# Kernel optimization log

Hardware: AMD Instinct MI355X
Metric: run time of the kernel (lower is better)

## Reference

```python
import jax, jax.numpy as jnp
import numpy as np

ANNEAL_T_START = 5.0
T_END = 1.0


def setup_inputs() -> dict:
    key = jax.random.key(0)
    ks = jax.random.split(key, 8)
    B, V, H, CD, WID = 8192, 1024, 128, 16, 64
    return {
        "cond": jax.random.normal(ks[0], (B, CD), jnp.float32),
        "W": 0.01 * jax.random.normal(ks[1], (V, H), jnp.float32),
        "b": 0.01 * jax.random.normal(ks[2], (V,), jnp.float32),
        "c": 0.01 * jax.random.normal(ks[3], (H,), jnp.float32),
        "fc1_w": jax.random.normal(ks[4], (WID, CD), jnp.float32) / np.float32(np.sqrt(CD)),
        "fc1_b": jnp.zeros((WID,), jnp.float32),
        "fc2_w": jax.random.normal(ks[5], (2 * (V + H), WID), jnp.float32) / np.float32(np.sqrt(WID)),
        "fc2_b": jnp.zeros((2 * (V + H),), jnp.float32),
        "falloff": jnp.float32(1.0),
        "steps": 16,
    }


def _bern(key, p):
    # Bernoulli sample as float of same dtype as p.
    return (jax.random.uniform(key, p.shape, p.dtype) < p).astype(p.dtype)


def reference(cond, W, b, c, fc1_w, fc1_b, fc2_w, fc2_b, falloff, steps):
    V, H = W.shape
    B = cond.shape[0]
    dtype = W.dtype

    # Conditioner: FiLM-style modulation of visible/hidden biases.
    x = jnp.tanh(cond @ fc1_w.T + fc1_b)
    x = x @ fc2_w.T + fc2_b  # [B, 2*(V+H)]
    gamma_b = x[:, :V]
    beta_b = x[:, V:2 * V]
    gamma_c = x[:, 2 * V:2 * V + H]
    beta_c = x[:, 2 * V + H:]
    b_mod = (1.0 + gamma_b) * b + beta_b  # [B, V]
    c_mod = (1.0 + gamma_c) * c + beta_c  # [B, H]
    bsum = jnp.sum(b_mod, axis=-1)  # [B], constant across steps

    # Annealing temperature schedule (sigmoid falloff).
    t = jnp.arange(steps, dtype=dtype)
    s = 1.0 / (1.0 + jnp.exp(falloff * (t - steps / 2.0)))
    temps = T_END + (ANNEAL_T_START - T_END) * s  # [steps]

    base = jax.random.key(42)
    v0 = _bern(jax.random.fold_in(base, 2 ** 20), jnp.full((B, V), 0.5, dtype))
    s0_0 = jnp.ones((B, 1), dtype)

    def flip(v, s0):
        return s0 * v + (1.0 - s0) * (1.0 - v)

    def step(carry, xs):
        v, s0 = carry
        i, T = xs
        k1, k2, k3 = jax.random.split(jax.random.fold_in(base, i), 3)
        v_eff = flip(v, s0)
        p_h = jax.nn.sigmoid((v_eff @ W + c_mod) / T)  # [B, H]
        h = _bern(k1, p_h)
        a = h @ W.T  # [B, V]
        vb = jnp.sum(v * b_mod, axis=-1)
        va = jnp.sum(v * a, axis=-1)
        dE = -bsum - jnp.sum(a, axis=-1) + 2.0 * vb + 2.0 * va  # [B]
        p_s0 = jax.nn.sigmoid(dE / T)
        s0n = _bern(k2, p_s0)[:, None]  # [B, 1]
        p_v = jax.nn.sigmoid((a + b_mod) / T)
        v_samp = _bern(k3, p_v)
        v_next = flip(v_samp, s0n)
        return (v_next, s0n), None

    (v, _), _ = jax.lax.scan(
        step, (v0, s0_0), (jnp.arange(steps, dtype=jnp.int32), temps)
    )
    return v
```

## Files before the change

kernel.cpp:

```cpp
#include <hip/hip_runtime.h>
#include <stdint.h>

#pragma clang fp contract(off)

#define B_ 8192
#define V_ 1024
#define H_ 128
#define CD_ 16
#define WID_ 64
#define NOUT_ 2304
#define STEPS_ 16

typedef float f32x2 __attribute__((ext_vector_type(2)));

__device__ __forceinline__ void pkfma(f32x2& acc, f32x2 wv, f32x2 bf2) {
  asm("v_pk_fma_f32 %0, %1, %2, %0" : "+v"(acc) : "v"(wv), "v"(bf2));
}

__host__ __device__ __forceinline__ void tf2x32(uint32_t k0, uint32_t k1,
                                                uint32_t x0, uint32_t x1,
                                                uint32_t* o0, uint32_t* o1) {
  uint32_t ks2 = k0 ^ k1 ^ 0x1BD11BDAu;
#define RL_(v, d) (((v) << (d)) | ((v) >> (32 - (d))))
#define RND_(a) { x0 += x1; x1 = RL_(x1, a); x1 ^= x0; }
  x0 += k0; x1 += k1;
  RND_(13) RND_(15) RND_(26) RND_(6)
  x0 += k1; x1 += ks2 + 1u;
  RND_(17) RND_(29) RND_(16) RND_(24)
  x0 += ks2; x1 += k0 + 2u;
  RND_(13) RND_(15) RND_(26) RND_(6)
  x0 += k0; x1 += k1 + 3u;
  RND_(17) RND_(29) RND_(16) RND_(24)
  x0 += k1; x1 += ks2 + 4u;
  RND_(13) RND_(15) RND_(26) RND_(6)
  x0 += ks2; x1 += k0 + 5u;
#undef RND_
#undef RL_
  *o0 = x0; *o1 = x1;
}

struct Keys { uint32_t a[6]; };

__device__ __forceinline__ uint32_t draw_bits(uint32_t ka, uint32_t kb, uint32_t j) {
  uint32_t x0, x1;
  tf2x32(ka, kb, 0u, j, &x0, &x1);
  return x0 ^ x1;
}

__device__ __forceinline__ float bits_to_u(uint32_t bits) {
  return __fsub_rn(__uint_as_float((bits >> 9) | 0x3f800000u), 1.0f);
}

__device__ __forceinline__ float exp_a(float x) {
  float xc = fminf(fmaxf(x, -88.3762626647949f), 88.3762626647950f);
  float fx = floorf(__fadd_rn(__fmul_rn(xc, 1.44269504088896341f), 0.5f));
  float xr = __fsub_rn(xc, __fmul_rn(0.693359375f, fx));
  xr = __fsub_rn(xr, __fmul_rn(-2.12194440e-4f, fx));
  float zz = __fmul_rn(xr, xr);
  float y = 1.9875691500E-4f;
  y = __fadd_rn(__fmul_rn(y, xr), 1.3981999507E-3f);
  y = __fadd_rn(__fmul_rn(y, xr), 8.3334519073E-3f);
  y = __fadd_rn(__fmul_rn(y, xr), 4.1665795894E-2f);
  y = __fadd_rn(__fmul_rn(y, xr), 1.6666665459E-1f);
  y = __fadd_rn(__fmul_rn(y, xr), 5.0000001201E-1f);
  y = __fadd_rn(__fmul_rn(y, zz), xr);
  y = __fadd_rn(y, 1.0f);
  int n = (int)fx;
  float sc = __int_as_float((n + 127) << 23);
  return __fmul_rn(y, sc);
}

__device__ __forceinline__ float tanh_a(float xin) {
  float x = fmaxf(fminf(xin, 7.90531110763549805f), -7.90531110763549805f);
  float x2 = __fmul_rn(x, x);
  float p = __fadd_rn(__fmul_rn(x2, -2.76076847742355e-16f), 2.00018790482477e-13f);
  p = __fadd_rn(__fmul_rn(x2, p), -8.60467152213735e-11f);
  p = __fadd_rn(__fmul_rn(x2, p), 5.12229709037114e-08f);
  p = __fadd_rn(__fmul_rn(x2, p), 1.48572235717979e-05f);
  p = __fadd_rn(__fmul_rn(x2, p), 6.37261928875436e-04f);
  p = __fadd_rn(__fmul_rn(x2, p), 4.89352455891786e-03f);
  p = __fmul_rn(x, p);
  float q = __fadd_rn(__fmul_rn(x2, 1.19825839466702e-06f), 1.18534705686654e-04f);
  q = __fadd_rn(__fmul_rn(x2, q), 2.26843463243900e-03f);
  q = __fadd_rn(__fmul_rn(x2, q), 4.89352518554385e-03f);
  float r = p / q;
  if (fabsf(xin) < 0.0004f) r = xin;
  return r;
}

__device__ __forceinline__ float sigmoid_a(float z) {
  float e = exp_a(-z);
  return 1.0f / __fadd_rn(1.0f, e);
}

__global__ void k_transpose(const float* __restrict__ W, float* __restrict__ WT,
                            const float* __restrict__ fc2w, float* __restrict__ fc2T) {
  int i = blockIdx.x * blockDim.x + threadIdx.x;
  if (i < V_ * H_) { int v = i / H_, h = i % H_; WT[h * V_ + v] = W[i]; }
  if (i < NOUT_ * WID_) { int j = i / WID_, w = i % WID_; fc2T[w * NOUT_ + j] = fc2w[i]; }
}

__global__ void k_temps(const float* __restrict__ falloff, float* __restrict__ temps) {
  int t = threadIdx.x;
  if (t < 16) {
    float arg = __fmul_rn(*falloff, __fsub_rn((float)t, 8.0f));
    float e = exp_a(arg);
    float s = 1.0f / __fadd_rn(1.0f, e);
    temps[t] = __fadd_rn(1.0f, __fmul_rn(4.0f, s));
  }
}

__global__ void k_mlp1(const float* __restrict__ cond, const float* __restrict__ fc1w,
                       const float* __restrict__ fc1b, float* __restrict__ xout) {
  int idx = blockIdx.x * blockDim.x + threadIdx.x;
  if (idx >= B_ * WID_) return;
  int row = idx >> 6, w = idx & 63;
  float acc = 0.0f;
  for (int k = 0; k < CD_; k++) acc = __fmaf_rn(cond[row * CD_ + k], fc1w[w * CD_ + k], acc);
  float z = __fadd_rn(acc, fc1b[w]);
  xout[idx] = tanh_a(z);
}

__global__ __launch_bounds__(128) void k_mlp2b(const float* __restrict__ xmlp,
                       const float* __restrict__ fc2T, const float* __restrict__ fc2b,
                       const float* __restrict__ bvec, float* __restrict__ b_mod) {
  __shared__ float xs[32][WID_];
  int jbase = blockIdx.x * 128;
  int r0 = blockIdx.y * 32;
  int tid = threadIdx.x;
  for (int t = tid; t < 32 * WID_; t += 128)
    xs[t >> 6][t & 63] = xmlp[(r0 + (t >> 6)) * WID_ + (t & 63)];
  __syncthreads();
  int j = jbase + tid;
  float accg[32], accb[32];
#pragma unroll
  for (int r = 0; r < 32; r++) { accg[r] = 0.0f; accb[r] = 0.0f; }
  for (int w = 0; w < WID_; w++) {
    float fg = fc2T[w * NOUT_ + j];
    float fb = fc2T[w * NOUT_ + 1024 + j];
#pragma unroll
    for (int r = 0; r < 32; r++) {
      float xv = xs[r][w];
      accg[r] = __fmaf_rn(xv, fg, accg[r]);
      accb[r] = __fmaf_rn(xv, fb, accb[r]);
    }
  }
  float bj = bvec[j];
  float biasg = fc2b[j], biasb = fc2b[1024 + j];
#pragma unroll
  for (int r = 0; r < 32; r++) {
    float g = __fadd_rn(accg[r], biasg);
    float bb = __fadd_rn(accb[r], biasb);
    float t1 = __fadd_rn(1.0f, g);
    b_mod[(r0 + r) * V_ + j] = __fadd_rn(__fmul_rn(t1, bj), bb);
  }
}

__global__ __launch_bounds__(128) void k_mlp2c(const float* __restrict__ xmlp,
                       const float* __restrict__ fc2T, const float* __restrict__ fc2b,
                       const float* __restrict__ cvec, float* __restrict__ c_mod) {
  __shared__ float xs[32][WID_];
  int r0 = blockIdx.y * 32;
  int tid = threadIdx.x;
  for (int t = tid; t < 32 * WID_; t += 128)
    xs[t >> 6][t & 63] = xmlp[(r0 + (t >> 6)) * WID_ + (t & 63)];
  __syncthreads();
  float accg[32], accb[32];
#pragma unroll
  for (int r = 0; r < 32; r++) { accg[r] = 0.0f; accb[r] = 0.0f; }
  for (int w = 0; w < WID_; w++) {
    float fg = fc2T[w * NOUT_ + 2048 + tid];
    float fb = fc2T[w * NOUT_ + 2176 + tid];
#pragma unroll
    for (int r = 0; r < 32; r++) {
      float xv = xs[r][w];
      accg[r] = __fmaf_rn(xv, fg, accg[r]);
      accb[r] = __fmaf_rn(xv, fb, accb[r]);
    }
  }
  float cj = cvec[tid];
  float biasg = fc2b[2048 + tid], biasb = fc2b[2176 + tid];
#pragma unroll
  for (int r = 0; r < 32; r++) {
    float g = __fadd_rn(accg[r], biasg);
    float bb = __fadd_rn(accb[r], biasb);
    float t1 = __fadd_rn(1.0f, g);
    c_mod[(r0 + r) * H_ + tid] = __fadd_rn(__fmul_rn(t1, cj), bb);
  }
}

__global__ __launch_bounds__(64) void k_bsum(const float* __restrict__ b_mod,
                                             float* __restrict__ bsum) {
  int row = blockIdx.x * 64 + threadIdx.x;
  const float4* bp = (const float4*)(b_mod + (size_t)row * V_);
  float acc = 0.0f;
  for (int c = 0; c < 32; c++) {
    float4 Bv[8];
#pragma unroll
    for (int q = 0; q < 8; q++) Bv[q] = bp[c * 8 + q];
#pragma unroll
    for (int q = 0; q < 8; q++) {
      acc = __fadd_rn(acc, Bv[q].x);
      acc = __fadd_rn(acc, Bv[q].y);
      acc = __fadd_rn(acc, Bv[q].z);
      acc = __fadd_rn(acc, Bv[q].w);
    }
  }
  bsum[row] = acc;
}

__global__ void k_v0(float* __restrict__ vout, uint32_t* __restrict__ v_bits,
                     float* __restrict__ s0, uint32_t kva, uint32_t kvb) {
  int idx = blockIdx.x * blockDim.x + threadIdx.x;
  int row = idx >> 10, col = idx & 1023;
  uint32_t bits = draw_bits(kva, kvb, (uint32_t)idx);
  float u = bits_to_u(bits);
  float v = (u < 0.5f) ? 1.0f : 0.0f;
  vout[idx] = v;
  unsigned long long m = __ballot(v == 1.0f);
  if ((threadIdx.x & 63) == 0) {
    v_bits[row * 32 + (col >> 5)] = (uint32_t)m;
    v_bits[row * 32 + (col >> 5) + 1] = (uint32_t)(m >> 32);
  }
  if (col == 0) s0[row] = 1.0f;
}

__global__ __launch_bounds__(256) void k_h(const float* __restrict__ W,
                   const float* __restrict__ c_mod, const uint32_t* __restrict__ v_bits,
                   const float* __restrict__ s0, uint32_t* __restrict__ h_bits,
                   const float* __restrict__ temps, int step, Keys kn) {
  __shared__ uint32_t nib[16][32];
  int tid = threadIdx.x;
  int ct = tid & 31;
  int rt = tid >> 5;
  int h0 = ct << 2;
  int row0 = blockIdx.x * 16 + rt * 2;
  float T = temps[step];
  f32x2 a00 = {0.f, 0.f}, a01 = {0.f, 0.f};
  f32x2 a10 = {0.f, 0.f}, a11 = {0.f, 0.f};
  uint32_t flip0 = (s0[row0] == 0.0f) ? 0xFFFFFFFFu : 0u;
  uint32_t flip1 = (s0[row0 + 1] == 0.0f) ? 0xFFFFFFFFu : 0u;
  const float* wp = W + h0;
  const uint4* vb0q = (const uint4*)(v_bits + (size_t)row0 * 32);
  const uint4* vb1q = (const uint4*)(v_bits + (size_t)(row0 + 1) * 32);

  float4 A[8], Bq[8];
  uint32_t m0, m1;
  auto LOADW = [&](float4* d, int kbase) {
#pragma unroll
    for (int i = 0; i < 8; i++)
      d[i] = *(const float4*)(wp + (size_t)(kbase + i) * H_);
  };
  auto DO8 = [&](const float4* wv) {
#pragma unroll
    for (int j = 0; j < 8; j++) {
      uint32_t s0m = (uint32_t)((int32_t)m0 >> 31); m0 <<= 1;
      uint32_t s1m = (uint32_t)((int32_t)m1 >> 31); m1 <<= 1;
      float bf0 = __uint_as_float(s0m & 0x3f800000u);
      float bf1 = __uint_as_float(s1m & 0x3f800000u);
      f32x2 wlo = {wv[j].x, wv[j].y};
      f32x2 whi = {wv[j].z, wv[j].w};
      f32x2 b0 = {bf0, bf0};
      f32x2 b1 = {bf1, bf1};
      pkfma(a00, wlo, b0); pkfma(a01, whi, b0);
      pkfma(a10, wlo, b1); pkfma(a11, whi, b1);
    }
  };

  uint4 q0 = vb0q[0], q1 = vb1q[0];
  uint4 q0n, q1n;
  LOADW(A, 0);
  for (int kq = 0; kq < 8; kq++) {
    if (kq < 7) { q0n = vb0q[kq + 1]; q1n = vb1q[kq + 1]; }
    const uint32_t w0s[4] = {q0.x, q0.y, q0.z, q0.w};
    const uint32_t w1s[4] = {q1.x, q1.y, q1.z, q1.w};
#pragma unroll
    for (int wq = 0; wq < 4; wq++) {
      int kb = kq * 128 + wq * 32;
      m0 = __brev(w0s[wq]) ^ flip0;
      m1 = __brev(w1s[wq]) ^ flip1;
      LOADW(Bq, kb + 8);  DO8(A);
      LOADW(A, kb + 16);  DO8(Bq);
      LOADW(Bq, kb + 24); DO8(A);
      if (kb + 32 < 1024) LOADW(A, kb + 32);
      DO8(Bq);
    }
    q0 = q0n; q1 = q1n;
  }

  const f32x2* accs[2][2] = {{&a00, &a01}, {&a10, &a11}};
#pragma unroll
  for (int r = 0; r < 2; r++) {
    int row = row0 + r;
    float4 cm = *(const float4*)(c_mod + (size_t)row * H_ + h0);
    const float cma[4] = {cm.x, cm.y, cm.z, cm.w};
    const float ac[4] = {(*accs[r][0])[0], (*accs[r][0])[1],
                         (*accs[r][1])[0], (*accs[r][1])[1]};
    uint32_t nb = 0;
#pragma unroll
    for (int e = 0; e < 4; e++) {
      float z = __fadd_rn(ac[e], cma[e]) / T;
      float p = sigmoid_a(z);
      uint32_t b = draw_bits(kn.a[0], kn.a[1], (uint32_t)(row * H_ + h0 + e));
      if (bits_to_u(b) < p) nb |= 1u << e;
    }
    nib[rt * 2 + r][ct] = nb;
  }
  __syncthreads();
  if (tid < 64) {
    int rloc = tid >> 2, wq = tid & 3;
    uint32_t word = 0;
#pragma unroll
    for (int i = 0; i < 8; i++) word |= nib[rloc][wq * 8 + i] << (4 * i);
    h_bits[(size_t)(blockIdx.x * 16 + rloc) * 4 + wq] = word;
  }
}

__global__ __launch_bounds__(256) void k_a(const float* __restrict__ WT,
                   const uint32_t* __restrict__ h_bits, float* __restrict__ a) {
  int tid = threadIdx.x;
  int ct = tid & 63;
  int rt = tid >> 6;
  int v0 = blockIdx.x * 256 + (ct << 2);
  int r0 = blockIdx.y * 32 + rt * 8;
  f32x2 acc[8][2];
#pragma unroll
  for (int r = 0; r < 8; r++) { acc[r][0] = f32x2{0.f, 0.f}; acc[r][1] = f32x2{0.f, 0.f}; }
  uint4 hw[8];
#pragma unroll
  for (int r = 0; r < 8; r++) hw[r] = *(const uint4*)(h_bits + (size_t)(r0 + r) * 4);
  const float* wp0 = WT + v0;

  auto asect = [&](int WW, const uint32_t mwin[8]) {
    uint32_t m[8];
#pragma unroll
    for (int r = 0; r < 8; r++) m[r] = __brev(mwin[r]);
    const float* wp = wp0 + (size_t)(WW * 32) * V_;
    for (int j4 = 0; j4 < 8; j4++) {
#pragma unroll
      for (int jj = 0; jj < 4; jj++) {
        float4 wv = *(const float4*)(wp + (size_t)jj * V_);
        f32x2 wlo = {wv.x, wv.y};
        f32x2 whi = {wv.z, wv.w};
#pragma unroll
        for (int r = 0; r < 8; r++) {
          uint32_t sm = (uint32_t)((int32_t)m[r] >> 31);
          m[r] <<= 1;
          float bf = __uint_as_float(sm & 0x3f800000u);
          f32x2 b2 = {bf, bf};
          pkfma(acc[r][0], wlo, b2);
          pkfma(acc[r][1], whi, b2);
        }
      }
      wp += (size_t)4 * V_;
    }
  };

  {
    uint32_t mw[8];
#pragma unroll
    for (int r = 0; r < 8; r++) mw[r] = hw[r].x;
    asect(0, mw);
#pragma unroll
    for (int r = 0; r < 8; r++) mw[r] = hw[r].y;
    asect(1, mw);
#pragma unroll
    for (int r = 0; r < 8; r++) mw[r] = hw[r].z;
    asect(2, mw);
#pragma unroll
    for (int r = 0; r < 8; r++) mw[r] = hw[r].w;
    asect(3, mw);
  }

#pragma unroll
  for (int r = 0; r < 8; r++) {
    float4 o = make_float4(acc[r][0][0], acc[r][0][1], acc[r][1][0], acc[r][1][1]);
    *(float4*)(a + (size_t)(r0 + r) * V_ + v0) = o;
  }
}

__global__ __launch_bounds__(256) void k_s0(const float* __restrict__ a,
                     const float* __restrict__ b_mod, const float* __restrict__ bsum,
                     const uint32_t* __restrict__ v_bits, float* __restrict__ s0,
                     const float* __restrict__ temps, int step, Keys kn) {
  __shared__ float As[2][16][132];
  __shared__ float Bs[2][16][132];
  int tid = threadIdx.x;
  int r0 = blockIdx.x * 16;

  auto STAGE = [&](int buf, int c) {
#pragma unroll
    for (int i = 0; i < 2; i++) {
      int e = tid + i * 256;
      int r = e >> 5, c4 = e & 31;
      float4 av = *(const float4*)(a + (size_t)(r0 + r) * V_ + c * 128 + c4 * 4);
      float4 bv = *(const float4*)(b_mod + (size_t)(r0 + r) * V_ + c * 128 + c4 * 4);
      *(float4*)&As[buf][r][c4 * 4] = av;
      *(float4*)&Bs[buf][r][c4 * 4] = bv;
    }
  };

  float suma = 0.0f, vb = 0.0f, va = 0.0f;
  STAGE(0, 0);
  __syncthreads();
  for (int c = 0; c < 8; c++) {
    if (c < 7) STAGE((c + 1) & 1, c + 1);
    if (tid < 16) {
      int row = r0 + tid;
      uint4 mw = *(const uint4*)(v_bits + (size_t)row * 32 + c * 4);
      const uint32_t mm[4] = {mw.x, mw.y, mw.z, mw.w};
#pragma unroll
      for (int w4 = 0; w4 < 4; w4++) {
        uint32_t m = mm[w4];
#pragma unroll
        for (int j4 = 0; j4 < 8; j4++) {
          float4 av4 = *(const float4*)&As[c & 1][tid][w4 * 32 + j4 * 4];
          float4 bv4 = *(const float4*)&Bs[c & 1][tid][w4 * 32 + j4 * 4];
          const float ax[4] = {av4.x, av4.y, av4.z, av4.w};
          const float bx[4] = {bv4.x, bv4.y, bv4.z, bv4.w};
#pragma unroll
          for (int e = 0; e < 4; e++) {
            float bit = (float)((m >> (j4 * 4 + e)) & 1u);
            suma = __fadd_rn(suma, ax[e]);
            vb = __fmaf_rn(bx[e], bit, vb);
            va = __fmaf_rn(ax[e], bit, va);
          }
        }
      }
    }
    __syncthreads();
  }
  if (tid < 16) {
    int row = r0 + tid;
    float dE = __fsub_rn(-bsum[row], suma);
    dE = __fadd_rn(dE, __fmul_rn(2.0f, vb));
    dE = __fadd_rn(dE, __fmul_rn(2.0f, va));
    float T = temps[step];
    float p = sigmoid_a(dE / T);
    uint32_t bits = draw_bits(kn.a[2], kn.a[3], (uint32_t)row);
    float u = bits_to_u(bits);
    s0[row] = (u < p) ? 1.0f : 0.0f;
  }
}

__global__ void k_v(const float* __restrict__ a, const float* __restrict__ b_mod,
                    const float* __restrict__ s0, float* __restrict__ vout,
                    uint32_t* __restrict__ v_bits, const float* __restrict__ temps, int step,
                    Keys kn) {
  int idx = blockIdx.x * blockDim.x + threadIdx.x;
  int row = idx >> 10, col = idx & 1023;
  float T = temps[step];
  float z = __fadd_rn(a[idx], b_mod[idx]) / T;
  float p = sigmoid_a(z);
  uint32_t bits = draw_bits(kn.a[4], kn.a[5], (uint32_t)idx);
  float u = bits_to_u(bits);
  float vs = (u < p) ? 1.0f : 0.0f;
  float vn = (s0[row] != 0.0f) ? vs : (1.0f - vs);
  vout[idx] = vn;
  unsigned long long m = __ballot(vn == 1.0f);
  if ((threadIdx.x & 63) == 0) {
    v_bits[row * 32 + (col >> 5)] = (uint32_t)m;
    v_bits[row * 32 + (col >> 5) + 1] = (uint32_t)(m >> 32);
  }
}

extern "C" void kernel_launch(void* const* d_in, const int* in_sizes, int n_in,
                              void* d_out, int out_size, void* d_ws, size_t ws_size,
                              hipStream_t stream) {
  const float* cond = (const float*)d_in[0];
  const float* W = (const float*)d_in[1];
  const float* bvec = (const float*)d_in[2];
  const float* cvec = (const float*)d_in[3];
  const float* fc1w = (const float*)d_in[4];
  const float* fc1b = (const float*)d_in[5];
  const float* fc2w = (const float*)d_in[6];
  const float* fc2b = (const float*)d_in[7];
  const float* falloff = (const float*)d_in[8];
  float* out = (float*)d_out;

  char* ws = (char*)d_ws;
  size_t off = 0;
  auto alloc = [&](size_t bytes) { void* p = ws + off; off += (bytes + 255) & ~(size_t)255; return p; };
  float* b_mod = (float*)alloc((size_t)B_ * V_ * 4);
  float* c_mod = (float*)alloc((size_t)B_ * H_ * 4);
  float* abuf  = (float*)alloc((size_t)B_ * V_ * 4);
  float* xmlp  = (float*)alloc((size_t)B_ * WID_ * 4);
  float* bsum  = (float*)alloc((size_t)B_ * 4);
  float* s0    = (float*)alloc((size_t)B_ * 4);
  uint32_t* v_bits = (uint32_t*)alloc((size_t)B_ * 32 * 4);
  uint32_t* h_bits = (uint32_t*)alloc((size_t)B_ * 4 * 4);
  float* WT    = (float*)alloc((size_t)H_ * V_ * 4);
  float* fc2T  = (float*)alloc((size_t)WID_ * NOUT_ * 4);
  float* temps = (float*)alloc(16 * 4);

  uint32_t kva, kvb;
  tf2x32(0u, 42u, 0u, 1048576u, &kva, &kvb);
  Keys kn[16];
  for (int i = 0; i < 16; i++) {
    uint32_t f0, f1;
    tf2x32(0u, 42u, 0u, (uint32_t)i, &f0, &f1);
    uint32_t a0, a1;
    tf2x32(f0, f1, 0u, 0u, &a0, &a1); kn[i].a[0] = a0; kn[i].a[1] = a1;
    tf2x32(f0, f1, 0u, 1u, &a0, &a1); kn[i].a[2] = a0; kn[i].a[3] = a1;
    tf2x32(f0, f1, 0u, 2u, &a0, &a1); kn[i].a[4] = a0; kn[i].a[5] = a1;
  }

  k_transpose<<<(NOUT_ * WID_ + 255) / 256, 256, 0, stream>>>(W, WT, fc2w, fc2T);
  k_temps<<<1, 64, 0, stream>>>(falloff, temps);
  k_mlp1<<<(B_ * WID_) / 256, 256, 0, stream>>>(cond, fc1w, fc1b, xmlp);
  k_mlp2b<<<dim3(8, 256), 128, 0, stream>>>(xmlp, fc2T, fc2b, bvec, b_mod);
  k_mlp2c<<<dim3(1, 256), 128, 0, stream>>>(xmlp, fc2T, fc2b, cvec, c_mod);
  k_bsum<<<B_ / 64, 64, 0, stream>>>(b_mod, bsum);
  k_v0<<<(B_ * V_) / 256, 256, 0, stream>>>(out, v_bits, s0, kva, kvb);

  for (int i = 0; i < STEPS_; i++) {
    k_h<<<B_ / 16, 256, 0, stream>>>(W, c_mod, v_bits, s0, h_bits, temps, i, kn[i]);
    k_a<<<dim3(4, B_ / 32), 256, 0, stream>>>(WT, h_bits, abuf);
    k_s0<<<B_ / 16, 256, 0, stream>>>(abuf, b_mod, bsum, v_bits, s0, temps, i, kn[i]);
    k_v<<<(B_ * V_) / 256, 256, 0, stream>>>(abuf, b_mod, s0, out, v_bits, temps, i, kn[i]);
  }
}
```

Measured before the change: 2.989 ms.

## Keep raw sampled visible bits, defer flip, write float output once

```diff
diff --git a/kernel.cpp b/kernel.cpp
--- a/kernel.cpp
+++ b/kernel.cpp
@@ -209,15 +209,13 @@
   bsum[row] = acc;
 }
 
-__global__ void k_v0(float* __restrict__ vout, uint32_t* __restrict__ v_bits,
-                     float* __restrict__ s0, uint32_t kva, uint32_t kvb) {
+__global__ void k_v0(uint32_t* __restrict__ v_bits, float* __restrict__ s0,
+                     uint32_t kva, uint32_t kvb) {
   int idx = blockIdx.x * blockDim.x + threadIdx.x;
   int row = idx >> 10, col = idx & 1023;
   uint32_t bits = draw_bits(kva, kvb, (uint32_t)idx);
   float u = bits_to_u(bits);
-  float v = (u < 0.5f) ? 1.0f : 0.0f;
-  vout[idx] = v;
-  unsigned long long m = __ballot(v == 1.0f);
+  unsigned long long m = __ballot(u < 0.5f);
   if ((threadIdx.x & 63) == 0) {
     v_bits[row * 32 + (col >> 5)] = (uint32_t)m;
     v_bits[row * 32 + (col >> 5) + 1] = (uint32_t)(m >> 32);
@@ -227,8 +225,8 @@
 
 __global__ __launch_bounds__(256) void k_h(const float* __restrict__ W,
                    const float* __restrict__ c_mod, const uint32_t* __restrict__ v_bits,
-                   const float* __restrict__ s0, uint32_t* __restrict__ h_bits,
-                   const float* __restrict__ temps, int step, Keys kn) {
+                   uint32_t* __restrict__ h_bits, const float* __restrict__ temps,
+                   int step, Keys kn) {
   __shared__ uint32_t nib[16][32];
   int tid = threadIdx.x;
   int ct = tid & 31;
@@ -238,13 +236,11 @@
   float T = temps[step];
   f32x2 a00 = {0.f, 0.f}, a01 = {0.f, 0.f};
   f32x2 a10 = {0.f, 0.f}, a11 = {0.f, 0.f};
-  uint32_t flip0 = (s0[row0] == 0.0f) ? 0xFFFFFFFFu : 0u;
-  uint32_t flip1 = (s0[row0 + 1] == 0.0f) ? 0xFFFFFFFFu : 0u;
   const float* wp = W + h0;
   const uint4* vb0q = (const uint4*)(v_bits + (size_t)row0 * 32);
   const uint4* vb1q = (const uint4*)(v_bits + (size_t)(row0 + 1) * 32);
 
-  float4 A[8], Bq[8];
+  float4 W0[8], W1[8], W2[8], W3[8];
   uint32_t m0, m1;
   auto LOADW = [&](float4* d, int kbase) {
 #pragma unroll
@@ -266,27 +262,34 @@
       pkfma(a10, wlo, b1); pkfma(a11, whi, b1);
     }
   };
+  auto WQ = [&](int kb, uint32_t mw0, uint32_t mw1, bool l0, bool l1, bool l2) {
+    m0 = __brev(mw0);
+    m1 = __brev(mw1);
+    LOADW(W3, kb + 24); DO8(W0);
+    if (l0) LOADW(W0, kb + 32);
+    DO8(W1);
+    if (l1) LOADW(W1, kb + 40);
+    DO8(W2);
+    if (l2) LOADW(W2, kb + 48);
+    DO8(W3);
+  };
 
   uint4 q0 = vb0q[0], q1 = vb1q[0];
   uint4 q0n, q1n;
-  LOADW(A, 0);
-  for (int kq = 0; kq < 8; kq++) {
-    if (kq < 7) { q0n = vb0q[kq + 1]; q1n = vb1q[kq + 1]; }
+  LOADW(W0, 0); LOADW(W1, 8); LOADW(W2, 16);
+  for (int kq = 0; kq < 7; kq++) {
+    q0n = vb0q[kq + 1]; q1n = vb1q[kq + 1];
     const uint32_t w0s[4] = {q0.x, q0.y, q0.z, q0.w};
     const uint32_t w1s[4] = {q1.x, q1.y, q1.z, q1.w};
 #pragma unroll
-    for (int wq = 0; wq < 4; wq++) {
-      int kb = kq * 128 + wq * 32;
-      m0 = __brev(w0s[wq]) ^ flip0;
-      m1 = __brev(w1s[wq]) ^ flip1;
-      LOADW(Bq, kb + 8);  DO8(A);
-      LOADW(A, kb + 16);  DO8(Bq);
-      LOADW(Bq, kb + 24); DO8(A);
-      if (kb + 32 < 1024) LOADW(A, kb + 32);
-      DO8(Bq);
-    }
+    for (int wq = 0; wq < 4; wq++)
+      WQ(kq * 128 + wq * 32, w0s[wq], w1s[wq], true, true, true);
     q0 = q0n; q1 = q1n;
   }
+  WQ(896, q0.x, q1.x, true, true, true);
+  WQ(928, q0.y, q1.y, true, true, true);
+  WQ(960, q0.z, q1.z, true, true, true);
+  WQ(992, q0.w, q1.w, false, false, false);
 
   const f32x2* accs[2][2] = {{&a00, &a01}, {&a10, &a11}};
 #pragma unroll
@@ -401,6 +404,8 @@
   };
 
   float suma = 0.0f, vb = 0.0f, va = 0.0f;
+  uint32_t flipm = 0;
+  if (tid < 16) flipm = (s0[r0 + tid] == 0.0f) ? 0xFFFFFFFFu : 0u;
   STAGE(0, 0);
   __syncthreads();
   for (int c = 0; c < 8; c++) {
@@ -408,7 +413,7 @@
     if (tid < 16) {
       int row = r0 + tid;
       uint4 mw = *(const uint4*)(v_bits + (size_t)row * 32 + c * 4);
-      const uint32_t mm[4] = {mw.x, mw.y, mw.z, mw.w};
+      const uint32_t mm[4] = {mw.x ^ flipm, mw.y ^ flipm, mw.z ^ flipm, mw.w ^ flipm};
 #pragma unroll
       for (int w4 = 0; w4 < 4; w4++) {
         uint32_t m = mm[w4];
@@ -444,9 +449,8 @@
 }
 
 __global__ void k_v(const float* __restrict__ a, const float* __restrict__ b_mod,
-                    const float* __restrict__ s0, float* __restrict__ vout,
-                    uint32_t* __restrict__ v_bits, const float* __restrict__ temps, int step,
-                    Keys kn) {
+                    uint32_t* __restrict__ v_bits, const float* __restrict__ temps,
+                    int step, Keys kn) {
   int idx = blockIdx.x * blockDim.x + threadIdx.x;
   int row = idx >> 10, col = idx & 1023;
   float T = temps[step];
@@ -454,14 +458,21 @@
   float p = sigmoid_a(z);
   uint32_t bits = draw_bits(kn.a[4], kn.a[5], (uint32_t)idx);
   float u = bits_to_u(bits);
-  float vs = (u < p) ? 1.0f : 0.0f;
-  float vn = (s0[row] != 0.0f) ? vs : (1.0f - vs);
-  vout[idx] = vn;
-  unsigned long long m = __ballot(vn == 1.0f);
+  unsigned long long m = __ballot(u < p);
   if ((threadIdx.x & 63) == 0) {
     v_bits[row * 32 + (col >> 5)] = (uint32_t)m;
     v_bits[row * 32 + (col >> 5) + 1] = (uint32_t)(m >> 32);
   }
+}
+
+__global__ void k_fin(const uint32_t* __restrict__ v_bits, const float* __restrict__ s0,
+                      float* __restrict__ vout) {
+  int idx = blockIdx.x * blockDim.x + threadIdx.x;
+  int row = idx >> 10, col = idx & 1023;
+  uint32_t w = v_bits[row * 32 + (col >> 5)];
+  uint32_t bit = (w >> (col & 31)) & 1u;
+  uint32_t eff = (s0[row] != 0.0f) ? bit : (bit ^ 1u);
+  vout[idx] = (float)eff;
 }
 
 extern "C" void kernel_launch(void* const* d_in, const int* in_sizes, int n_in,
@@ -511,12 +522,14 @@
   k_mlp2b<<<dim3(8, 256), 128, 0, stream>>>(xmlp, fc2T, fc2b, bvec, b_mod);
   k_mlp2c<<<dim3(1, 256), 128, 0, stream>>>(xmlp, fc2T, fc2b, cvec, c_mod);
   k_bsum<<<B_ / 64, 64, 0, stream>>>(b_mod, bsum);
-  k_v0<<<(B_ * V_) / 256, 256, 0, stream>>>(out, v_bits, s0, kva, kvb);
+  k_v0<<<(B_ * V_) / 256, 256, 0, stream>>>(v_bits, s0, kva, kvb);
 
   for (int i = 0; i < STEPS_; i++) {
-    k_h<<<B_ / 16, 256, 0, stream>>>(W, c_mod, v_bits, s0, h_bits, temps, i, kn[i]);
+    k_h<<<B_ / 16, 256, 0, stream>>>(W, c_mod, v_bits, h_bits, temps, i, kn[i]);
     k_a<<<dim3(4, B_ / 32), 256, 0, stream>>>(WT, h_bits, abuf);
     k_s0<<<B_ / 16, 256, 0, stream>>>(abuf, b_mod, bsum, v_bits, s0, temps, i, kn[i]);
-    k_v<<<(B_ * V_) / 256, 256, 0, stream>>>(abuf, b_mod, s0, out, v_bits, temps, i, kn[i]);
-  }
-}
+    k_v<<<(B_ * V_) / 256, 256, 0, stream>>>(abuf, b_mod, v_bits, temps, i, kn[i]);
+  }
+
+  k_fin<<<(B_ * V_) / 256, 256, 0, stream>>>(v_bits, s0, out);
+}
```

Result: slower. 3.674 ms (+22.9%).

## Fuse visible sampling into s0 kernel and defer flip to final expansion

Applied to the files above, without the earlier changes.

```diff
diff --git a/kernel.cpp b/kernel.cpp
--- a/kernel.cpp
+++ b/kernel.cpp
@@ -209,15 +209,13 @@
   bsum[row] = acc;
 }
 
-__global__ void k_v0(float* __restrict__ vout, uint32_t* __restrict__ v_bits,
-                     float* __restrict__ s0, uint32_t kva, uint32_t kvb) {
+__global__ void k_v0(uint32_t* __restrict__ v_bits, float* __restrict__ s0,
+                     uint32_t kva, uint32_t kvb) {
   int idx = blockIdx.x * blockDim.x + threadIdx.x;
   int row = idx >> 10, col = idx & 1023;
   uint32_t bits = draw_bits(kva, kvb, (uint32_t)idx);
   float u = bits_to_u(bits);
-  float v = (u < 0.5f) ? 1.0f : 0.0f;
-  vout[idx] = v;
-  unsigned long long m = __ballot(v == 1.0f);
+  unsigned long long m = __ballot(u < 0.5f);
   if ((threadIdx.x & 63) == 0) {
     v_bits[row * 32 + (col >> 5)] = (uint32_t)m;
     v_bits[row * 32 + (col >> 5) + 1] = (uint32_t)(m >> 32);
@@ -227,8 +225,8 @@
 
 __global__ __launch_bounds__(256) void k_h(const float* __restrict__ W,
                    const float* __restrict__ c_mod, const uint32_t* __restrict__ v_bits,
-                   const float* __restrict__ s0, uint32_t* __restrict__ h_bits,
-                   const float* __restrict__ temps, int step, Keys kn) {
+                   uint32_t* __restrict__ h_bits, const float* __restrict__ temps,
+                   int step, Keys kn) {
   __shared__ uint32_t nib[16][32];
   int tid = threadIdx.x;
   int ct = tid & 31;
@@ -238,8 +236,6 @@
   float T = temps[step];
   f32x2 a00 = {0.f, 0.f}, a01 = {0.f, 0.f};
   f32x2 a10 = {0.f, 0.f}, a11 = {0.f, 0.f};
-  uint32_t flip0 = (s0[row0] == 0.0f) ? 0xFFFFFFFFu : 0u;
-  uint32_t flip1 = (s0[row0 + 1] == 0.0f) ? 0xFFFFFFFFu : 0u;
   const float* wp = W + h0;
   const uint4* vb0q = (const uint4*)(v_bits + (size_t)row0 * 32);
   const uint4* vb1q = (const uint4*)(v_bits + (size_t)(row0 + 1) * 32);
@@ -277,8 +273,8 @@
 #pragma unroll
     for (int wq = 0; wq < 4; wq++) {
       int kb = kq * 128 + wq * 32;
-      m0 = __brev(w0s[wq]) ^ flip0;
-      m1 = __brev(w1s[wq]) ^ flip1;
+      m0 = __brev(w0s[wq]);
+      m1 = __brev(w1s[wq]);
       LOADW(Bq, kb + 8);  DO8(A);
       LOADW(A, kb + 16);  DO8(Bq);
       LOADW(Bq, kb + 24); DO8(A);
@@ -331,45 +327,41 @@
   for (int r = 0; r < 8; r++) hw[r] = *(const uint4*)(h_bits + (size_t)(r0 + r) * 4);
   const float* wp0 = WT + v0;
 
-  auto asect = [&](int WW, const uint32_t mwin[8]) {
-    uint32_t m[8];
-#pragma unroll
-    for (int r = 0; r < 8; r++) m[r] = __brev(mwin[r]);
-    const float* wp = wp0 + (size_t)(WW * 32) * V_;
-    for (int j4 = 0; j4 < 8; j4++) {
-#pragma unroll
-      for (int jj = 0; jj < 4; jj++) {
-        float4 wv = *(const float4*)(wp + (size_t)jj * V_);
-        f32x2 wlo = {wv.x, wv.y};
-        f32x2 whi = {wv.z, wv.w};
-#pragma unroll
-        for (int r = 0; r < 8; r++) {
-          uint32_t sm = (uint32_t)((int32_t)m[r] >> 31);
-          m[r] <<= 1;
-          float bf = __uint_as_float(sm & 0x3f800000u);
-          f32x2 b2 = {bf, bf};
-          pkfma(acc[r][0], wlo, b2);
-          pkfma(acc[r][1], whi, b2);
-        }
+  uint32_t m[8];
+  float4 buf0[4], buf1[4];
+  auto LOADG = [&](float4* d, int g) {
+    const float* wp = wp0 + (size_t)(g * 4) * V_;
+#pragma unroll
+    for (int jj = 0; jj < 4; jj++) d[jj] = *(const float4*)(wp + (size_t)jj * V_);
+  };
+  auto COMP = [&](const float4* d) {
+#pragma unroll
+    for (int jj = 0; jj < 4; jj++) {
+      f32x2 wlo = {d[jj].x, d[jj].y};
+      f32x2 whi = {d[jj].z, d[jj].w};
+#pragma unroll
+      for (int r = 0; r < 8; r++) {
+        uint32_t sm = (uint32_t)((int32_t)m[r] >> 31);
+        m[r] <<= 1;
+        float bf = __uint_as_float(sm & 0x3f800000u);
+        f32x2 b2 = {bf, bf};
+        pkfma(acc[r][0], wlo, b2);
+        pkfma(acc[r][1], whi, b2);
       }
-      wp += (size_t)4 * V_;
     }
   };
 
-  {
-    uint32_t mw[8];
-#pragma unroll
-    for (int r = 0; r < 8; r++) mw[r] = hw[r].x;
-    asect(0, mw);
-#pragma unroll
-    for (int r = 0; r < 8; r++) mw[r] = hw[r].y;
-    asect(1, mw);
-#pragma unroll
-    for (int r = 0; r < 8; r++) mw[r] = hw[r].z;
-    asect(2, mw);
-#pragma unroll
-    for (int r = 0; r < 8; r++) mw[r] = hw[r].w;
-    asect(3, mw);
+  LOADG(buf0, 0);
+#pragma unroll
+  for (int g = 0; g < 32; g++) {
+    if ((g & 7) == 0) {
+      const int s = g >> 3;
+#pragma unroll
+      for (int r = 0; r < 8; r++)
+        m[r] = __brev(s == 0 ? hw[r].x : s == 1 ? hw[r].y : s == 2 ? hw[r].z : hw[r].w);
+    }
+    if (g & 1) { if (g < 31) LOADG(buf0, g + 1); COMP(buf1); }
+    else       { if (g < 31) LOADG(buf1, g + 1); COMP(buf0); }
   }
 
 #pragma unroll
@@ -379,14 +371,18 @@
   }
 }
 
-__global__ __launch_bounds__(256) void k_s0(const float* __restrict__ a,
+__global__ __launch_bounds__(256) void k_sv(const float* __restrict__ a,
                      const float* __restrict__ b_mod, const float* __restrict__ bsum,
-                     const uint32_t* __restrict__ v_bits, float* __restrict__ s0,
-                     const float* __restrict__ temps, int step, Keys kn) {
+                     const uint32_t* __restrict__ vb_old, uint32_t* __restrict__ vb_new,
+                     float* __restrict__ s0, const float* __restrict__ temps,
+                     int step, Keys kn) {
   __shared__ float As[2][16][132];
   __shared__ float Bs[2][16][132];
   int tid = threadIdx.x;
   int r0 = blockIdx.x * 16;
+  float T = temps[step];
+  int wv = tid >> 6;
+  int lane = tid & 63;
 
   auto STAGE = [&](int buf, int c) {
 #pragma unroll
@@ -401,14 +397,35 @@
   };
 
   float suma = 0.0f, vb = 0.0f, va = 0.0f;
+  uint32_t flipm = 0;
+  if (tid < 16) flipm = (s0[r0 + tid] == 0.0f) ? 0xFFFFFFFFu : 0u;
   STAGE(0, 0);
   __syncthreads();
   for (int c = 0; c < 8; c++) {
     if (c < 7) STAGE((c + 1) & 1, c + 1);
+#pragma unroll
+    for (int i = 0; i < 8; i++) {
+      int e = tid + i * 256;
+      int rl = e >> 7, cl = e & 127;
+      float av = As[c & 1][rl][cl];
+      float bv = Bs[c & 1][rl][cl];
+      float z = __fadd_rn(av, bv) / T;
+      float p = sigmoid_a(z);
+      int row = r0 + rl;
+      int col = c * 128 + cl;
+      uint32_t bits = draw_bits(kn.a[4], kn.a[5], (uint32_t)(row * V_ + col));
+      float u = bits_to_u(bits);
+      unsigned long long mball = __ballot(u < p);
+      if (lane == 0) {
+        int base = row * 32 + (col >> 5);
+        vb_new[base] = (uint32_t)mball;
+        vb_new[base + 1] = (uint32_t)(mball >> 32);
+      }
+    }
     if (tid < 16) {
       int row = r0 + tid;
-      uint4 mw = *(const uint4*)(v_bits + (size_t)row * 32 + c * 4);
-      const uint32_t mm[4] = {mw.x, mw.y, mw.z, mw.w};
+      uint4 mw = *(const uint4*)(vb_old + (size_t)row * 32 + c * 4);
+      const uint32_t mm[4] = {mw.x ^ flipm, mw.y ^ flipm, mw.z ^ flipm, mw.w ^ flipm};
 #pragma unroll
       for (int w4 = 0; w4 < 4; w4++) {
         uint32_t m = mm[w4];
@@ -435,7 +452,6 @@
     float dE = __fsub_rn(-bsum[row], suma);
     dE = __fadd_rn(dE, __fmul_rn(2.0f, vb));
     dE = __fadd_rn(dE, __fmul_rn(2.0f, va));
-    float T = temps[step];
     float p = sigmoid_a(dE / T);
     uint32_t bits = draw_bits(kn.a[2], kn.a[3], (uint32_t)row);
     float u = bits_to_u(bits);
@@ -443,25 +459,14 @@
   }
 }
 
-__global__ void k_v(const float* __restrict__ a, const float* __restrict__ b_mod,
-                    const float* __restrict__ s0, float* __restrict__ vout,
-                    uint32_t* __restrict__ v_bits, const float* __restrict__ temps, int step,
-                    Keys kn) {
+__global__ void k_fin(const uint32_t* __restrict__ v_bits, const float* __restrict__ s0,
+                      float* __restrict__ vout) {
   int idx = blockIdx.x * blockDim.x + threadIdx.x;
   int row = idx >> 10, col = idx & 1023;
-  float T = temps[step];
-  float z = __fadd_rn(a[idx], b_mod[idx]) / T;
-  float p = sigmoid_a(z);
-  uint32_t bits = draw_bits(kn.a[4], kn.a[5], (uint32_t)idx);
-  float u = bits_to_u(bits);
-  float vs = (u < p) ? 1.0f : 0.0f;
-  float vn = (s0[row] != 0.0f) ? vs : (1.0f - vs);
-  vout[idx] = vn;
-  unsigned long long m = __ballot(vn == 1.0f);
-  if ((threadIdx.x & 63) == 0) {
-    v_bits[row * 32 + (col >> 5)] = (uint32_t)m;
-    v_bits[row * 32 + (col >> 5) + 1] = (uint32_t)(m >> 32);
-  }
+  uint32_t w = v_bits[row * 32 + (col >> 5)];
+  uint32_t bit = (w >> (col & 31)) & 1u;
+  uint32_t eff = (s0[row] != 0.0f) ? bit : (bit ^ 1u);
+  vout[idx] = (float)eff;
 }
 
 extern "C" void kernel_launch(void* const* d_in, const int* in_sizes, int n_in,
@@ -487,11 +492,13 @@
   float* xmlp  = (float*)alloc((size_t)B_ * WID_ * 4);
   float* bsum  = (float*)alloc((size_t)B_ * 4);
   float* s0    = (float*)alloc((size_t)B_ * 4);
-  uint32_t* v_bits = (uint32_t*)alloc((size_t)B_ * 32 * 4);
+  uint32_t* v_bits0 = (uint32_t*)alloc((size_t)B_ * 32 * 4);
+  uint32_t* v_bits1 = (uint32_t*)alloc((size_t)B_ * 32 * 4);
   uint32_t* h_bits = (uint32_t*)alloc((size_t)B_ * 4 * 4);
   float* WT    = (float*)alloc((size_t)H_ * V_ * 4);
   float* fc2T  = (float*)alloc((size_t)WID_ * NOUT_ * 4);
   float* temps = (float*)alloc(16 * 4);
+  uint32_t* vb[2] = {v_bits0, v_bits1};
 
   uint32_t kva, kvb;
   tf2x32(0u, 42u, 0u, 1048576u, &kva, &kvb);
@@ -511,12 +518,14 @@
   k_mlp2b<<<dim3(8, 256), 128, 0, stream>>>(xmlp, fc2T, fc2b, bvec, b_mod);
   k_mlp2c<<<dim3(1, 256), 128, 0, stream>>>(xmlp, fc2T, fc2b, cvec, c_mod);
   k_bsum<<<B_ / 64, 64, 0, stream>>>(b_mod, bsum);
-  k_v0<<<(B_ * V_) / 256, 256, 0, stream>>>(out, v_bits, s0, kva, kvb);
+  k_v0<<<(B_ * V_) / 256, 256, 0, stream>>>(vb[0], s0, kva, kvb);
 
   for (int i = 0; i < STEPS_; i++) {
-    k_h<<<B_ / 16, 256, 0, stream>>>(W, c_mod, v_bits, s0, h_bits, temps, i, kn[i]);
+    k_h<<<B_ / 16, 256, 0, stream>>>(W, c_mod, vb[i & 1], h_bits, temps, i, kn[i]);
     k_a<<<dim3(4, B_ / 32), 256, 0, stream>>>(WT, h_bits, abuf);
-    k_s0<<<B_ / 16, 256, 0, stream>>>(abuf, b_mod, bsum, v_bits, s0, temps, i, kn[i]);
-    k_v<<<(B_ * V_) / 256, 256, 0, stream>>>(abuf, b_mod, s0, out, v_bits, temps, i, kn[i]);
-  }
-}
+    k_sv<<<B_ / 16, 256, 0, stream>>>(abuf, b_mod, bsum, vb[i & 1], vb[(i + 1) & 1],
+                                      s0, temps, i, kn[i]);
+  }
+
+  k_fin<<<(B_ * V_) / 256, 256, 0, stream>>>(vb[0], s0, out);
+}
```

Result: no change. 2.986 ms (-0.1%).
